# Performance work log

Measured on AMD Instinct MI355X. Metric: run time of the kernel, lower is better.

Reference implementation:

```python
import jax, jax.numpy as jnp
import numpy as np

T, B, E, H, HID, SIG = 1024, 4, 1024, 16, 1024, 64


def setup_inputs() -> dict:
    key = jax.random.key(0)
    ks = jax.random.split(key, 16)
    sc = 0.02
    return {
        "x": jax.random.normal(ks[0], (T, B, E), jnp.float32),
        "Wq": jax.random.normal(ks[1], (E, E), jnp.float32) * sc,
        "bq": jnp.zeros((E,), jnp.float32),
        "Wk": jax.random.normal(ks[2], (E, E), jnp.float32) * sc,
        "bk": jnp.zeros((E,), jnp.float32),
        "Wv": jax.random.normal(ks[3], (E, E), jnp.float32) * sc,
        "bv": jnp.zeros((E,), jnp.float32),
        "Wo": jax.random.normal(ks[4], (E, E), jnp.float32) * sc,
        "bo": jnp.zeros((E,), jnp.float32),
        "W1": jax.random.normal(ks[5], (HID, E), jnp.float32) * sc,
        "b1": jnp.zeros((HID,), jnp.float32),
        "W2": jax.random.normal(ks[6], (SIG, HID), jnp.float32) * sc,
        "b2": jnp.zeros((SIG,), jnp.float32),
        "head_signatures": jax.random.normal(ks[7], (H, SIG), jnp.float32),
    }


def reference(x, Wq, bq, Wk, bk, Wv, bv, Wo, bo, W1, b1, W2, b2, head_signatures):
    # x: (T, B, E) fairseq layout; self-attention, no mask, eval mode (no dropout)
    T_, B_, E_ = x.shape
    H_ = head_signatures.shape[0]
    d = E_ // H_
    scaling = d ** -0.5

    q = (x @ Wq.T + bq) * scaling            # (T,B,E)
    k = x @ Wk.T + bk
    v = x @ Wv.T + bv

    def split_heads(z):                        # (T,B,E) -> (B,H,T,d)
        return z.reshape(T_, B_, H_, d).transpose(1, 2, 0, 3)

    qh, kh, vh = split_heads(q), split_heads(k), split_heads(v)

    scores = jnp.einsum("bhtd,bhsd->bhts", qh, kh)   # (B,H,T,T)
    attn = jax.nn.softmax(scores, axis=-1)
    o = jnp.einsum("bhts,bhsd->bhtd", attn, vh)      # (B,H,T,d)

    # head-competition gate: signature MLP on x, match against head signatures,
    # softmax over heads ('softmax' competition type)
    t = jax.nn.relu(x @ W1.T + b1) @ W2.T + b2       # (T,B,SIG)
    logits = t @ head_signatures.T                   # (T,B,H)
    gate = jax.nn.softmax(logits, axis=-1)
    gate = gate.transpose(1, 2, 0)                   # (B,H,T)

    o = o * gate[..., None]                          # gate per-head outputs
    out = o.transpose(2, 0, 1, 3).reshape(T_, B_, E_)  # (T,B,E)
    return out @ Wo.T + bo
```

## Files before the change

### kernel.cpp

```cpp
#include <hip/hip_runtime.h>

#define Tn   1024
#define Bn   4
#define En   1024
#define Hn   16
#define HIDn 1024
#define SIGn 64
#define Mn   (Tn * Bn)

typedef short  s8x8  __attribute__((ext_vector_type(8)));
typedef float  f32x4 __attribute__((ext_vector_type(4)));

__device__ __forceinline__ unsigned short f2bf(float f) {
    unsigned int x = __float_as_uint(f);
    unsigned int r = (x + 0x7fffu + ((x >> 16) & 1u)) >> 16;
    return (unsigned short)r;
}
__device__ __forceinline__ float exp2asm(float x) {
    float r;
    asm("v_exp_f32 %0, %1" : "=v"(r) : "v"(x));
    return r;
}
__device__ __forceinline__ unsigned int cvtpk(float a, float b) {
    unsigned int r;
    asm("v_cvt_pk_bf16_f32 %0, %1, %2" : "=v"(r) : "v"(a), "v"(b));
    return r;
}

__device__ __forceinline__ void gload_lds16(const void* g, void* l) {
    __builtin_amdgcn_global_load_lds(
        (const __attribute__((address_space(1))) unsigned int*)g,
        (__attribute__((address_space(3))) unsigned int*)l, 16, 0, 0);
}

__device__ __forceinline__ void cast8(const float* s, unsigned short* d) {
    const float4* p = (const float4*)s;
    float4 a = p[0], b = p[1];
    s8x8 o;
    o[0] = (short)f2bf(a.x); o[1] = (short)f2bf(a.y);
    o[2] = (short)f2bf(a.z); o[3] = (short)f2bf(a.w);
    o[4] = (short)f2bf(b.x); o[5] = (short)f2bf(b.y);
    o[6] = (short)f2bf(b.z); o[7] = (short)f2bf(b.w);
    *(s8x8*)d = o;
}

__global__ __launch_bounds__(256) void prep_all(
    const float* __restrict__ x,  const float* __restrict__ W1,
    const float* __restrict__ Wq, const float* __restrict__ Wk,
    const float* __restrict__ Wv, const float* __restrict__ W2,
    const float* __restrict__ b1, const float* __restrict__ bq,
    const float* __restrict__ bk, const float* __restrict__ bv,
    unsigned short* __restrict__ Wcat, unsigned short* __restrict__ W2b,
    float* __restrict__ bcat, unsigned short* __restrict__ xb, int pre)
{
    const size_t WELEM = (size_t)En * En;
    const int y = blockIdx.y, bx = blockIdx.x, tid = threadIdx.x;
    if (y < 4) {
        const float* src = (y == 0) ? W1 : (y == 1) ? Wq : (y == 2) ? Wk : Wv;
        size_t i = (size_t)bx * 256 + tid;
        cast8(src + i * 8, Wcat + y * WELEM + i * 8);
    } else if (y == 4) {
        if (bx < 32) {
            size_t i = (size_t)bx * 256 + tid;
            cast8(W2 + i * 8, W2b + i * 8);
        } else if (bx < 48) {
            int idx = (bx - 32) * 256 + tid;
            int w = idx >> 10;
            const float* s = (w == 0) ? b1 : (w == 1) ? bq : (w == 2) ? bk : bv;
            bcat[idx] = s[idx & 1023];
        }
    } else {
        if (!pre) return;
        int q = y - 5;
        size_t i = (size_t)bx * 256 + tid;
        cast8(x + q * WELEM + i * 8, xb + q * WELEM + i * 8);
    }
}

template <int PRE>
__global__ __launch_bounds__(256) void fused_proj(
    const float* __restrict__ X, const unsigned short* __restrict__ Xb,
    const unsigned short* __restrict__ Wcat, const float* __restrict__ bcat,
    unsigned short* __restrict__ t1b, unsigned short* __restrict__ qb,
    unsigned short* __restrict__ kb, unsigned short* __restrict__ vb)
{
    __shared__ __align__(16) short As[128 * 32];
    __shared__ __align__(16) short Bs[128 * 32];
    const int tid  = threadIdx.x;
    const int wave = tid >> 6;
    const int lane = tid & 63;
    const int ln15 = lane & 15;
    const int kq   = lane >> 4;
    const int wr   = wave >> 1;
    const int wc   = wave & 1;
    const int bn   = blockIdx.x;
    const int bm   = blockIdx.y;
    const size_t rowA0 = (size_t)bm * 128;
    const size_t rowB0 = (size_t)bn * 128;

    const int lrow   = lane >> 2;
    const int lchunk = lane & 3;

    f32x4 acc[4][4];
#pragma unroll
    for (int m = 0; m < 4; m++)
#pragma unroll
        for (int n = 0; n < 4; n++) acc[m][n] = (f32x4){0.f, 0.f, 0.f, 0.f};

    for (int k0 = 0; k0 < 1024; k0 += 32) {
#pragma unroll
        for (int i = 0; i < 2; i++) {
            int row = wave * 32 + i * 16 + lrow;
            int c   = lchunk ^ ((row >> 1) & 3);
            gload_lds16(Wcat + (rowB0 + row) * 1024 + k0 + c * 8,
                        &Bs[(wave * 32 + i * 16) * 32]);
        }
        if (PRE) {
#pragma unroll
            for (int i = 0; i < 2; i++) {
                int row = wave * 32 + i * 16 + lrow;
                int c   = lchunk ^ ((row >> 1) & 3);
                gload_lds16(Xb + (rowA0 + row) * 1024 + k0 + c * 8,
                            &As[(wave * 32 + i * 16) * 32]);
            }
        } else {
            const int srow = tid >> 1;
            const int scol = (tid & 1) * 16;
            const float4* src = (const float4*)(X + (rowA0 + srow) * 1024 + k0 + scol);
            float4 a = src[0], b = src[1], c4 = src[2], d4 = src[3];
            s8x8 v0, v1;
            v0[0] = (short)f2bf(a.x);  v0[1] = (short)f2bf(a.y);
            v0[2] = (short)f2bf(a.z);  v0[3] = (short)f2bf(a.w);
            v0[4] = (short)f2bf(b.x);  v0[5] = (short)f2bf(b.y);
            v0[6] = (short)f2bf(b.z);  v0[7] = (short)f2bf(b.w);
            v1[0] = (short)f2bf(c4.x); v1[1] = (short)f2bf(c4.y);
            v1[2] = (short)f2bf(c4.z); v1[3] = (short)f2bf(c4.w);
            v1[4] = (short)f2bf(d4.x); v1[5] = (short)f2bf(d4.y);
            v1[6] = (short)f2bf(d4.z); v1[7] = (short)f2bf(d4.w);
            int sw = (srow >> 1) & 3;
            int c0 = (scol >> 3) ^ sw;
            int c1 = ((scol >> 3) + 1) ^ sw;
            *(s8x8*)&As[srow * 32 + c0 * 8] = v0;
            *(s8x8*)&As[srow * 32 + c1 * 8] = v1;
        }
        asm volatile("s_waitcnt vmcnt(0)" ::: "memory");
        __syncthreads();

        s8x8 af[4], bf[4];
#pragma unroll
        for (int m = 0; m < 4; m++) {
            int row = wr * 64 + m * 16 + ln15;
            af[m] = *(const s8x8*)&As[row * 32 + (kq ^ ((row >> 1) & 3)) * 8];
        }
#pragma unroll
        for (int n = 0; n < 4; n++) {
            int row = wc * 64 + n * 16 + ln15;
            bf[n] = *(const s8x8*)&Bs[row * 32 + (kq ^ ((row >> 1) & 3)) * 8];
        }
#pragma unroll
        for (int m = 0; m < 4; m++)
#pragma unroll
            for (int n = 0; n < 4; n++)
                acc[m][n] = __builtin_amdgcn_mfma_f32_16x16x32_bf16(
                    af[m], bf[n], acc[m][n], 0, 0, 0);
        __syncthreads();
    }

    const int which = bn >> 3;
    unsigned short* dst = (which == 0) ? t1b : (which == 1) ? qb
                        : (which == 2) ? kb : vb;
    const float scale = (which == 1) ? 0.18033688011112042f : 1.0f;
    const int   relu  = (which == 0);
    const int   cbase = (bn & 7) * 128;

    float bcol[4];
#pragma unroll
    for (int n = 0; n < 4; n++)
        bcol[n] = bcat[bn * 128 + wc * 64 + n * 16 + ln15];
#pragma unroll
    for (int m = 0; m < 4; m++) {
        size_t gr0 = rowA0 + wr * 64 + m * 16 + kq * 4;
#pragma unroll
        for (int n = 0; n < 4; n++) {
            int gc = cbase + wc * 64 + n * 16 + ln15;
#pragma unroll
            for (int j = 0; j < 4; j++) {
                float vv = acc[m][n][j] + bcol[n];
                if (relu) vv = fmaxf(vv, 0.f);
                vv *= scale;
                dst[(gr0 + j) * 1024 + gc] = f2bf(vv);
            }
        }
    }
}

__global__ __launch_bounds__(256) void out_proj(
    const unsigned short* __restrict__ A, const unsigned short* __restrict__ W,
    const float* __restrict__ bias, float* __restrict__ C)
{
    __shared__ __align__(16) short As[64 * 32];
    __shared__ __align__(16) short Bs[128 * 32];
    const int tid  = threadIdx.x;
    const int wave = tid >> 6;
    const int lane = tid & 63;
    const int ln15 = lane & 15;
    const int kq   = lane >> 4;
    const int wr   = wave >> 1;
    const int wc   = wave & 1;
    const size_t rowA0 = (size_t)blockIdx.y * 64;
    const size_t rowB0 = (size_t)blockIdx.x * 128;

    const int lrow   = lane >> 2;
    const int lchunk = lane & 3;

    f32x4 acc[2][4];
#pragma unroll
    for (int m = 0; m < 2; m++)
#pragma unroll
        for (int n = 0; n < 4; n++) acc[m][n] = (f32x4){0.f, 0.f, 0.f, 0.f};

    for (int k0 = 0; k0 < 1024; k0 += 32) {
        {
            int row = wave * 16 + lrow;
            int c   = lchunk ^ ((row >> 1) & 3);
            gload_lds16(A + (rowA0 + row) * 1024 + k0 + c * 8,
                        &As[(wave * 16) * 32]);
        }
#pragma unroll
        for (int i = 0; i < 2; i++) {
            int row = wave * 32 + i * 16 + lrow;
            int c   = lchunk ^ ((row >> 1) & 3);
            gload_lds16(W + (rowB0 + row) * 1024 + k0 + c * 8,
                        &Bs[(wave * 32 + i * 16) * 32]);
        }
        asm volatile("s_waitcnt vmcnt(0)" ::: "memory");
        __syncthreads();

        s8x8 af[2], bf[4];
#pragma unroll
        for (int m = 0; m < 2; m++) {
            int row = wr * 32 + m * 16 + ln15;
            af[m] = *(const s8x8*)&As[row * 32 + (kq ^ ((row >> 1) & 3)) * 8];
        }
#pragma unroll
        for (int n = 0; n < 4; n++) {
            int row = wc * 64 + n * 16 + ln15;
            bf[n] = *(const s8x8*)&Bs[row * 32 + (kq ^ ((row >> 1) & 3)) * 8];
        }
#pragma unroll
        for (int m = 0; m < 2; m++)
#pragma unroll
            for (int n = 0; n < 4; n++)
                acc[m][n] = __builtin_amdgcn_mfma_f32_16x16x32_bf16(
                    af[m], bf[n], acc[m][n], 0, 0, 0);
        __syncthreads();
    }

    float bcol[4];
#pragma unroll
    for (int n = 0; n < 4; n++)
        bcol[n] = bias[rowB0 + wc * 64 + n * 16 + ln15];
#pragma unroll
    for (int m = 0; m < 2; m++) {
        size_t gr0 = rowA0 + wr * 32 + m * 16 + kq * 4;
#pragma unroll
        for (int n = 0; n < 4; n++) {
            size_t gc = rowB0 + wc * 64 + n * 16 + ln15;
#pragma unroll
            for (int j = 0; j < 4; j++)
                C[(gr0 + j) * 1024 + gc] = acc[m][n][j] + bcol[n];
        }
    }
}

__global__ __launch_bounds__(256) void t2gate(
    const unsigned short* __restrict__ t1, const unsigned short* __restrict__ W2b,
    const float* __restrict__ b2, const float* __restrict__ hs,
    float* __restrict__ gate)
{
    __shared__ __align__(16) short As[16 * 64];
    __shared__ __align__(16) short Bs[64 * 64];
    __shared__ float t2s[16][65];
    __shared__ float hss[16][65];
    const int tid   = threadIdx.x;
    const int wave  = tid >> 6;
    const int lane  = tid & 63;
    const int ln15  = lane & 15;
    const int kq    = lane >> 4;
    const int lrow8 = lane >> 3;
    const int lch   = lane & 7;
    const int m0    = blockIdx.x * 16;

    {
        int r = tid >> 4, c = (tid & 15) * 4;
        float4 v = *(const float4*)(hs + r * 64 + c);
        hss[r][c] = v.x; hss[r][c + 1] = v.y; hss[r][c + 2] = v.z; hss[r][c + 3] = v.w;
    }

    f32x4 acc = (f32x4){0.f, 0.f, 0.f, 0.f};
    for (int k0 = 0; k0 < 1024; k0 += 64) {
        if (wave < 2) {
            int row = wave * 8 + lrow8;
            int cg  = lch ^ (row & 7);
            gload_lds16(t1 + (size_t)(m0 + row) * 1024 + k0 + cg * 8,
                        &As[(wave * 8) * 64]);
        }
#pragma unroll
        for (int i = 0; i < 2; i++) {
            int row = wave * 16 + i * 8 + lrow8;
            int cg  = lch ^ (row & 7);
            gload_lds16(W2b + (size_t)row * 1024 + k0 + cg * 8,
                        &Bs[(wave * 16 + i * 8) * 64]);
        }
        asm volatile("s_waitcnt vmcnt(0)" ::: "memory");
        __syncthreads();

#pragma unroll
        for (int kk = 0; kk < 2; kk++) {
            int arow = ln15;
            int brow = wave * 16 + ln15;
            s8x8 af = *(const s8x8*)&As[arow * 64 + (((kk * 4 + kq) ^ (arow & 7)) * 8)];
            s8x8 bf = *(const s8x8*)&Bs[brow * 64 + (((kk * 4 + kq) ^ (brow & 7)) * 8)];
            acc = __builtin_amdgcn_mfma_f32_16x16x32_bf16(af, bf, acc, 0, 0, 0);
        }
        __syncthreads();
    }

#pragma unroll
    for (int j = 0; j < 4; j++)
        t2s[kq * 4 + j][wave * 16 + ln15] = acc[j] + b2[wave * 16 + ln15];
    __syncthreads();

    int r = tid >> 4, hd = tid & 15;
    float s = 0.f;
#pragma unroll 16
    for (int d = 0; d < 64; d++) s += t2s[r][d] * hss[hd][d];
    float mx = s;
    mx = fmaxf(mx, __shfl_xor(mx, 1));
    mx = fmaxf(mx, __shfl_xor(mx, 2));
    mx = fmaxf(mx, __shfl_xor(mx, 4));
    mx = fmaxf(mx, __shfl_xor(mx, 8));
    float e = __expf(s - mx);
    float sum = e;
    sum += __shfl_xor(sum, 1);
    sum += __shfl_xor(sum, 2);
    sum += __shfl_xor(sum, 4);
    sum += __shfl_xor(sum, 8);
    gate[(size_t)(m0 + r) * Hn + hd] = e / sum;
}

__global__ __launch_bounds__(256) void trans_wo(
    const unsigned short* __restrict__ vb, unsigned short* __restrict__ vt,
    const float* __restrict__ Wo, unsigned short* __restrict__ Wob)
{
    const int bx = blockIdx.x, tid = threadIdx.x;
    if (bx >= 1024) {
        size_t i = (size_t)(bx - 1024) * 256 + tid;
        cast8(Wo + i * 8, Wob + i * 8);
        return;
    }
    __shared__ unsigned short ts[64][65];
    const int bh = bx & 63;
    const int b = bh >> 4, h = bh & 15;
    const int t0 = (bx >> 6) * 64;
    {
        int tr = tid >> 2, dq = (tid & 3) * 16;
        const unsigned short* src =
            vb + ((size_t)(t0 + tr) * Bn + b) * En + h * 64 + dq;
        s8x8 a = *(const s8x8*)src;
        s8x8 c = *(const s8x8*)(src + 8);
#pragma unroll
        for (int i = 0; i < 8; i++) {
            ts[tr][dq + i]     = (unsigned short)a[i];
            ts[tr][dq + 8 + i] = (unsigned short)c[i];
        }
    }
    __syncthreads();
    {
        int dr = tid >> 2, tq = (tid & 3) * 16;
        unsigned short* dst = vt + ((size_t)bh * 64 + dr) * Tn + t0 + tq;
        s8x8 o0, o1;
#pragma unroll
        for (int i = 0; i < 8; i++) {
            o0[i] = (short)ts[tq + i][dr];
            o1[i] = (short)ts[tq + 8 + i][dr];
        }
        *(s8x8*)dst = o0;
        *(s8x8*)(dst + 8) = o1;
    }
}

__global__ __launch_bounds__(512, 2) void attn_mfma(
    const unsigned short* __restrict__ q, const unsigned short* __restrict__ k,
    const unsigned short* __restrict__ vt, const float* __restrict__ gate,
    unsigned short* __restrict__ o)
{
    __shared__ __align__(16) short Kls[2][64 * 64];
    __shared__ __align__(16) short Vls[2][64 * 64];

    const int tid  = threadIdx.x;
    const int w    = tid >> 6;
    const int lane = tid & 63;
    const int ln   = lane & 15;
    const int kq   = lane >> 4;
    const int bh   = blockIdx.x;
    const int b    = bh >> 4;
    const int h    = bh & 15;
    const int qt   = blockIdx.y;

    s8x8 qf[2];
    {
        const int qrow = qt * 128 + w * 16 + ln;
        const unsigned short* src =
            q + ((size_t)qrow * Bn + b) * En + h * 64 + kq * 8;
        qf[0] = *(const s8x8*)(src);
        qf[1] = *(const s8x8*)(src + 32);
    }

    f32x4 OT[4];
#pragma unroll
    for (int n = 0; n < 4; n++) OT[n] = (f32x4){0.f, 0.f, 0.f, 0.f};
    float mrun = -1e30f, lrun = 0.f;

    const int srow = w * 8 + (lane >> 3);
    const int sch  = (lane & 7) ^ (srow & 7);
    const int sn  = srow >> 4;
    const int sK0 = 32 * (sn >> 1) + 4 * (sn & 1)
                  + 8 * ((srow >> 2) & 3) + (srow & 3);

    auto stage = [&](int bufi, int s0) {
        const unsigned short* gk =
            k + ((size_t)(s0 + sK0) * Bn + b) * En + h * 64 + sch * 8;
        gload_lds16(gk, &Kls[bufi][w * 512]);
        const unsigned short* gv =
            vt + ((size_t)bh * 64 + srow) * Tn + s0 + sch * 8;
        gload_lds16(gv, &Vls[bufi][w * 512]);
    };

    stage(0, 0);
    asm volatile("s_waitcnt vmcnt(0)" ::: "memory");
    __syncthreads();

    int cur = 0;
    for (int t = 0; t < Tn / 64; t++) {
        if (t + 1 < Tn / 64) stage(cur ^ 1, (t + 1) * 64);

        f32x4 S[4];
        __builtin_amdgcn_s_setprio(1);
#pragma unroll
        for (int n = 0; n < 4; n++) {
            S[n] = (f32x4){0.f, 0.f, 0.f, 0.f};
#pragma unroll
            for (int kk = 0; kk < 2; kk++) {
                int row = n * 16 + ln;
                int cc  = (kk * 4 + kq) ^ (row & 7);
                s8x8 kf = *(const s8x8*)&Kls[cur][row * 64 + cc * 8];
                S[n] = __builtin_amdgcn_mfma_f32_16x16x32_bf16(kf, qf[kk], S[n], 0, 0, 0);
            }
        }
        __builtin_amdgcn_s_setprio(0);

        float rm;
        {
            f32x4 t0 = S[0];
#pragma unroll
            for (int n = 1; n < 4; n++) {
                t0[0] = fmaxf(t0[0], S[n][0]); t0[1] = fmaxf(t0[1], S[n][1]);
                t0[2] = fmaxf(t0[2], S[n][2]); t0[3] = fmaxf(t0[3], S[n][3]);
            }
            rm = fmaxf(fmaxf(t0[0], t0[1]), fmaxf(t0[2], t0[3]));
            rm = fmaxf(rm, __shfl_xor(rm, 16));
            rm = fmaxf(rm, __shfl_xor(rm, 32));
        }

        if (__any(rm > mrun + 8.0f)) {
            float mnew = fmaxf(mrun, rm);
            float fs = exp2asm(mrun - mnew);
            lrun *= fs;
#pragma unroll
            for (int n = 0; n < 4; n++) {
                OT[n][0] *= fs; OT[n][1] *= fs; OT[n][2] *= fs; OT[n][3] *= fs;
            }
            mrun = mnew;
        }

        float ps = 0.f;
#pragma unroll
        for (int n = 0; n < 4; n++) {
            S[n][0] = exp2asm(S[n][0] - mrun); ps += S[n][0];
            S[n][1] = exp2asm(S[n][1] - mrun); ps += S[n][1];
            S[n][2] = exp2asm(S[n][2] - mrun); ps += S[n][2];
            S[n][3] = exp2asm(S[n][3] - mrun); ps += S[n][3];
        }
        ps += __shfl_xor(ps, 16);
        ps += __shfl_xor(ps, 32);
        lrun += ps;

        union { unsigned int u[4]; s8x8 v; } pb[2];
#pragma unroll
        for (int kk = 0; kk < 2; kk++) {
            pb[kk].u[0] = cvtpk(S[2 * kk][0],     S[2 * kk][1]);
            pb[kk].u[1] = cvtpk(S[2 * kk][2],     S[2 * kk][3]);
            pb[kk].u[2] = cvtpk(S[2 * kk + 1][0], S[2 * kk + 1][1]);
            pb[kk].u[3] = cvtpk(S[2 * kk + 1][2], S[2 * kk + 1][3]);
        }

        __builtin_amdgcn_s_setprio(1);
#pragma unroll
        for (int kk = 0; kk < 2; kk++) {
#pragma unroll
            for (int n = 0; n < 4; n++) {
                int row = n * 16 + ln;
                int cv  = (kk * 4 + kq) ^ (row & 7);
                s8x8 vf = *(const s8x8*)&Vls[cur][row * 64 + cv * 8];
                OT[n] = __builtin_amdgcn_mfma_f32_16x16x32_bf16(vf, pb[kk].v, OT[n], 0, 0, 0);
            }
        }
        __builtin_amdgcn_s_setprio(0);

        asm volatile("s_waitcnt vmcnt(0)" ::: "memory");
        __syncthreads();
        cur ^= 1;
    }

    {
        int tq = qt * 128 + w * 16 + ln;
        size_t m = (size_t)tq * Bn + b;
        float g = gate[m * Hn + h] / lrun;
        unsigned short* dst = o + m * En + h * 64;
#pragma unroll
        for (int n = 0; n < 4; n++) {
            int d0 = n * 16 + kq * 4;
            uint2 pkv;
            pkv.x = cvtpk(OT[n][0] * g, OT[n][1] * g);
            pkv.y = cvtpk(OT[n][2] * g, OT[n][3] * g);
            *(uint2*)(dst + d0) = pkv;
        }
    }
}

extern "C" void kernel_launch(void* const* d_in, const int* in_sizes, int n_in,
                              void* d_out, int out_size, void* d_ws, size_t ws_size,
                              hipStream_t stream)
{
    const float* x  = (const float*)d_in[0];
    const float* Wq = (const float*)d_in[1];
    const float* bq = (const float*)d_in[2];
    const float* Wk = (const float*)d_in[3];
    const float* bk = (const float*)d_in[4];
    const float* Wv = (const float*)d_in[5];
    const float* bv = (const float*)d_in[6];
    const float* Wo = (const float*)d_in[7];
    const float* bo = (const float*)d_in[8];
    const float* W1 = (const float*)d_in[9];
    const float* b1 = (const float*)d_in[10];
    const float* W2 = (const float*)d_in[11];
    const float* b2 = (const float*)d_in[12];
    const float* hs = (const float*)d_in[13];

    const size_t WELEM = (size_t)En * En;
    unsigned short* Wcat = (unsigned short*)d_ws;
    unsigned short* W2b  = Wcat + 4 * WELEM;
    float* bcat = (float*)(W2b + (size_t)SIGn * HIDn);
    float* gate = bcat + 4096;
    unsigned short* t1b = (unsigned short*)(gate + (size_t)Mn * Hn);
    unsigned short* qb  = t1b + (size_t)Mn * En;
    unsigned short* kb  = qb  + (size_t)Mn * En;
    unsigned short* vb  = kb  + (size_t)Mn * En;
    unsigned short* xb  = vb  + (size_t)Mn * En;
    unsigned short* Wob = Wcat;
    unsigned short* vtb = t1b;
    unsigned short* ob  = vb;

    const size_t need_xb =
        (size_t)((char*)(xb + (size_t)Mn * En) - (char*)d_ws);
    const bool pre = ws_size >= need_xb;

    dim3 blk(256);

    prep_all<<<dim3(512, 9), blk, 0, stream>>>(
        x, W1, Wq, Wk, Wv, W2, b1, bq, bk, bv, Wcat, W2b, bcat, xb, (int)pre);

    if (pre) {
        fused_proj<1><<<dim3(32, 32), blk, 0, stream>>>(
            x, xb, Wcat, bcat, t1b, qb, kb, vb);
    } else {
        fused_proj<0><<<dim3(32, 32), blk, 0, stream>>>(
            x, xb, Wcat, bcat, t1b, qb, kb, vb);
    }

    t2gate<<<dim3(Mn / 16), blk, 0, stream>>>(t1b, W2b, b2, hs, gate);

    trans_wo<<<dim3(1536), blk, 0, stream>>>(vb, vtb, Wo, Wob);

    attn_mfma<<<dim3(Bn * Hn, Tn / 128), dim3(512), 0, stream>>>(
        qb, kb, vtb, gate, ob);

    out_proj<<<dim3(En / 128, Mn / 64), blk, 0, stream>>>(ob, Wob, bo, (float*)d_out);
}
```

Measured before the change: 124.3 us.

## Pipeline projection GEMM with per-wave double-buffered LDS and merge mid-stage kernels

```diff
diff --git a/kernel.cpp b/kernel.cpp
--- a/kernel.cpp
+++ b/kernel.cpp
@@ -77,9 +77,136 @@
     }
 }
 
-template <int PRE>
-__global__ __launch_bounds__(256) void fused_proj(
-    const float* __restrict__ X, const unsigned short* __restrict__ Xb,
+__global__ __launch_bounds__(256) void fused_proj_pipe(
+    const unsigned short* __restrict__ Xb,
+    const unsigned short* __restrict__ Wcat, const float* __restrict__ bcat,
+    unsigned short* __restrict__ t1b, unsigned short* __restrict__ qb,
+    unsigned short* __restrict__ kb, unsigned short* __restrict__ vb)
+{
+    __shared__ __align__(16) short Ls[4][2][2][64 * 32];
+    const int tid  = threadIdx.x;
+    const int wave = tid >> 6;
+    const int lane = tid & 63;
+    const int ln15 = lane & 15;
+    const int kq   = lane >> 4;
+    const int wr   = wave >> 1;
+    const int wc   = wave & 1;
+    const int bn   = blockIdx.x;
+    const int bm   = blockIdx.y;
+    const size_t rowA0 = (size_t)bm * 128;
+    const size_t rowB0 = (size_t)bn * 128;
+
+    const int lr = lane >> 2;
+    const int lc = lane & 3;
+    const unsigned short* pa[4];
+    const unsigned short* pb[4];
+#pragma unroll
+    for (int i = 0; i < 4; i++) {
+        int r = i * 16 + lr;
+        int c = lc ^ ((r >> 1) & 3);
+        pa[i] = Xb   + (rowA0 + wr * 64 + r) * 1024 + c * 8;
+        pb[i] = Wcat + (rowB0 + wc * 64 + r) * 1024 + c * 8;
+    }
+    short* lA0 = &Ls[wave][0][0][0];
+    short* lA1 = &Ls[wave][1][0][0];
+    short* lB0 = &Ls[wave][0][1][0];
+    short* lB1 = &Ls[wave][1][1][0];
+
+    f32x4 acc[4][4];
+#pragma unroll
+    for (int m = 0; m < 4; m++)
+#pragma unroll
+        for (int n = 0; n < 4; n++) acc[m][n] = (f32x4){0.f, 0.f, 0.f, 0.f};
+
+    const int rsw = (kq ^ ((ln15 >> 1) & 3)) * 8;
+
+#define STAGE(lA, lB)                                          \
+    do {                                                       \
+        _Pragma("unroll")                                      \
+        for (int i = 0; i < 4; i++)                            \
+            gload_lds16(pa[i], (lA) + i * 16 * 32);            \
+        _Pragma("unroll")                                      \
+        for (int i = 0; i < 4; i++)                            \
+            gload_lds16(pb[i], (lB) + i * 16 * 32);            \
+        _Pragma("unroll")                                      \
+        for (int i = 0; i < 4; i++) { pa[i] += 32; pb[i] += 32; } \
+    } while (0)
+
+#define COMPUTE(lA, lB)                                                   \
+    do {                                                                  \
+        s8x8 af[4], bf4[4];                                               \
+        _Pragma("unroll")                                                 \
+        for (int m = 0; m < 4; m++)                                       \
+            af[m] = *(const s8x8*)((lA) + (m * 16 + ln15) * 32 + rsw);    \
+        _Pragma("unroll")                                                 \
+        for (int n = 0; n < 4; n++)                                       \
+            bf4[n] = *(const s8x8*)((lB) + (n * 16 + ln15) * 32 + rsw);   \
+        _Pragma("unroll")                                                 \
+        for (int m = 0; m < 4; m++)                                       \
+            _Pragma("unroll")                                             \
+            for (int n = 0; n < 4; n++)                                   \
+                acc[m][n] = __builtin_amdgcn_mfma_f32_16x16x32_bf16(      \
+                    af[m], bf4[n], acc[m][n], 0, 0, 0);                   \
+    } while (0)
+
+    STAGE(lA0, lB0);
+    STAGE(lA1, lB1);
+
+    for (int t = 0; t < 28; t += 2) {
+        asm volatile("s_waitcnt vmcnt(8)" ::: "memory");
+        COMPUTE(lA0, lB0);
+        asm volatile("s_waitcnt lgkmcnt(0)" ::: "memory");
+        STAGE(lA0, lB0);
+        asm volatile("s_waitcnt vmcnt(8)" ::: "memory");
+        COMPUTE(lA1, lB1);
+        asm volatile("s_waitcnt lgkmcnt(0)" ::: "memory");
+        STAGE(lA1, lB1);
+    }
+    asm volatile("s_waitcnt vmcnt(8)" ::: "memory");
+    COMPUTE(lA0, lB0);
+    asm volatile("s_waitcnt lgkmcnt(0)" ::: "memory");
+    STAGE(lA0, lB0);
+    asm volatile("s_waitcnt vmcnt(8)" ::: "memory");
+    COMPUTE(lA1, lB1);
+    asm volatile("s_waitcnt lgkmcnt(0)" ::: "memory");
+    STAGE(lA1, lB1);
+    asm volatile("s_waitcnt vmcnt(8)" ::: "memory");
+    COMPUTE(lA0, lB0);
+    asm volatile("s_waitcnt vmcnt(0)" ::: "memory");
+    COMPUTE(lA1, lB1);
+#undef STAGE
+#undef COMPUTE
+
+    const int which = bn >> 3;
+    unsigned short* dst = (which == 0) ? t1b : (which == 1) ? qb
+                        : (which == 2) ? kb : vb;
+    const float scale = (which == 1) ? 0.18033688011112042f : 1.0f;
+    const int   relu  = (which == 0);
+    const int   cbase = (bn & 7) * 128;
+
+    float bcol[4];
+#pragma unroll
+    for (int n = 0; n < 4; n++)
+        bcol[n] = bcat[bn * 128 + wc * 64 + n * 16 + ln15];
+#pragma unroll
+    for (int m = 0; m < 4; m++) {
+        size_t gr0 = rowA0 + wr * 64 + m * 16 + kq * 4;
+#pragma unroll
+        for (int n = 0; n < 4; n++) {
+            int gc = cbase + wc * 64 + n * 16 + ln15;
+#pragma unroll
+            for (int j = 0; j < 4; j++) {
+                float vv = acc[m][n][j] + bcol[n];
+                if (relu) vv = fmaxf(vv, 0.f);
+                vv *= scale;
+                dst[(gr0 + j) * 1024 + gc] = f2bf(vv);
+            }
+        }
+    }
+}
+
+__global__ __launch_bounds__(256) void fused_proj_fb(
+    const float* __restrict__ X,
     const unsigned short* __restrict__ Wcat, const float* __restrict__ bcat,
     unsigned short* __restrict__ t1b, unsigned short* __restrict__ qb,
     unsigned short* __restrict__ kb, unsigned short* __restrict__ vb)
@@ -97,7 +224,6 @@
     const int bm   = blockIdx.y;
     const size_t rowA0 = (size_t)bm * 128;
     const size_t rowB0 = (size_t)bn * 128;
-
     const int lrow   = lane >> 2;
     const int lchunk = lane & 3;
 
@@ -115,15 +241,7 @@
             gload_lds16(Wcat + (rowB0 + row) * 1024 + k0 + c * 8,
                         &Bs[(wave * 32 + i * 16) * 32]);
         }
-        if (PRE) {
-#pragma unroll
-            for (int i = 0; i < 2; i++) {
-                int row = wave * 32 + i * 16 + lrow;
-                int c   = lchunk ^ ((row >> 1) & 3);
-                gload_lds16(Xb + (rowA0 + row) * 1024 + k0 + c * 8,
-                            &As[(wave * 32 + i * 16) * 32]);
-            }
-        } else {
+        {
             const int srow = tid >> 1;
             const int scol = (tid & 1) * 16;
             const float4* src = (const float4*)(X + (rowA0 + srow) * 1024 + k0 + scol);
@@ -209,7 +327,6 @@
     const int wc   = wave & 1;
     const size_t rowA0 = (size_t)blockIdx.y * 64;
     const size_t rowB0 = (size_t)blockIdx.x * 128;
-
     const int lrow   = lane >> 2;
     const int lchunk = lane & 3;
 
@@ -273,23 +390,20 @@
     }
 }
 
-__global__ __launch_bounds__(256) void t2gate(
+__device__ __forceinline__ void t2gate_body(
+    int blk, int tid,
     const unsigned short* __restrict__ t1, const unsigned short* __restrict__ W2b,
     const float* __restrict__ b2, const float* __restrict__ hs,
-    float* __restrict__ gate)
-{
-    __shared__ __align__(16) short As[16 * 64];
-    __shared__ __align__(16) short Bs[64 * 64];
-    __shared__ float t2s[16][65];
-    __shared__ float hss[16][65];
-    const int tid   = threadIdx.x;
+    float* __restrict__ gate,
+    short* As, short* Bs, float (*t2s)[65], float (*hss)[65])
+{
     const int wave  = tid >> 6;
     const int lane  = tid & 63;
     const int ln15  = lane & 15;
     const int kq    = lane >> 4;
     const int lrow8 = lane >> 3;
     const int lch   = lane & 7;
-    const int m0    = blockIdx.x * 16;
+    const int m0    = blk * 16;
 
     {
         int r = tid >> 4, c = (tid & 15) * 4;
@@ -303,14 +417,14 @@
             int row = wave * 8 + lrow8;
             int cg  = lch ^ (row & 7);
             gload_lds16(t1 + (size_t)(m0 + row) * 1024 + k0 + cg * 8,
-                        &As[(wave * 8) * 64]);
+                        As + (wave * 8) * 64);
         }
 #pragma unroll
         for (int i = 0; i < 2; i++) {
             int row = wave * 16 + i * 8 + lrow8;
             int cg  = lch ^ (row & 7);
             gload_lds16(W2b + (size_t)row * 1024 + k0 + cg * 8,
-                        &Bs[(wave * 16 + i * 8) * 64]);
+                        Bs + (wave * 16 + i * 8) * 64);
         }
         asm volatile("s_waitcnt vmcnt(0)" ::: "memory");
         __syncthreads();
@@ -319,8 +433,8 @@
         for (int kk = 0; kk < 2; kk++) {
             int arow = ln15;
             int brow = wave * 16 + ln15;
-            s8x8 af = *(const s8x8*)&As[arow * 64 + (((kk * 4 + kq) ^ (arow & 7)) * 8)];
-            s8x8 bf = *(const s8x8*)&Bs[brow * 64 + (((kk * 4 + kq) ^ (brow & 7)) * 8)];
+            s8x8 af = *(const s8x8*)(As + arow * 64 + (((kk * 4 + kq) ^ (arow & 7)) * 8));
+            s8x8 bf = *(const s8x8*)(Bs + brow * 64 + (((kk * 4 + kq) ^ (brow & 7)) * 8));
             acc = __builtin_amdgcn_mfma_f32_16x16x32_bf16(af, bf, acc, 0, 0, 0);
         }
         __syncthreads();
@@ -349,20 +463,12 @@
     gate[(size_t)(m0 + r) * Hn + hd] = e / sum;
 }
 
-__global__ __launch_bounds__(256) void trans_wo(
+__device__ __forceinline__ void vtrans_body(
+    int bh, int t0, int tid,
     const unsigned short* __restrict__ vb, unsigned short* __restrict__ vt,
-    const float* __restrict__ Wo, unsigned short* __restrict__ Wob)
-{
-    const int bx = blockIdx.x, tid = threadIdx.x;
-    if (bx >= 1024) {
-        size_t i = (size_t)(bx - 1024) * 256 + tid;
-        cast8(Wo + i * 8, Wob + i * 8);
-        return;
-    }
-    __shared__ unsigned short ts[64][65];
-    const int bh = bx & 63;
+    unsigned short (*ts)[65])
+{
     const int b = bh >> 4, h = bh & 15;
-    const int t0 = (bx >> 6) * 64;
     {
         int tr = tid >> 2, dq = (tid & 3) * 16;
         const unsigned short* src =
@@ -387,6 +493,55 @@
         }
         *(s8x8*)dst = o0;
         *(s8x8*)(dst + 8) = o1;
+    }
+}
+
+__global__ __launch_bounds__(256) void t2gate_k(
+    const unsigned short* __restrict__ t1, const unsigned short* __restrict__ W2b,
+    const float* __restrict__ b2, const float* __restrict__ hs,
+    float* __restrict__ gate)
+{
+    __shared__ __align__(16) short As[16 * 64];
+    __shared__ __align__(16) short Bs[64 * 64];
+    __shared__ float t2s[16][65];
+    __shared__ float hss[16][65];
+    t2gate_body(blockIdx.x, threadIdx.x, t1, W2b, b2, hs, gate, As, Bs, t2s, hss);
+}
+__global__ __launch_bounds__(256) void trans_wo_k(
+    const unsigned short* __restrict__ vb, unsigned short* __restrict__ vt,
+    const float* __restrict__ Wo, unsigned short* __restrict__ Wob)
+{
+    const int bx = blockIdx.x, tid = threadIdx.x;
+    if (bx >= 1024) {
+        size_t i = (size_t)(bx - 1024) * 256 + tid;
+        cast8(Wo + i * 8, Wob + i * 8);
+        return;
+    }
+    __shared__ unsigned short ts[64][65];
+    vtrans_body(bx & 63, (bx >> 6) * 64, tid, vb, vt, ts);
+}
+
+__global__ __launch_bounds__(256) void midstage(
+    const unsigned short* __restrict__ t1, const unsigned short* __restrict__ W2b,
+    const float* __restrict__ b2, const float* __restrict__ hs,
+    float* __restrict__ gate,
+    const unsigned short* __restrict__ vb, unsigned short* __restrict__ vt,
+    const float* __restrict__ Wo, unsigned short* __restrict__ Wob)
+{
+    __shared__ __align__(16) short As[16 * 64];
+    __shared__ __align__(16) short Bs[64 * 64];
+    __shared__ float t2s[16][65];
+    __shared__ float hss[16][65];
+    __shared__ unsigned short ts[64][65];
+    const int bx = blockIdx.x, tid = threadIdx.x;
+    if (bx < 256) {
+        t2gate_body(bx, tid, t1, W2b, b2, hs, gate, As, Bs, t2s, hss);
+    } else if (bx < 1280) {
+        int v = bx - 256;
+        vtrans_body(v & 63, (v >> 6) * 64, tid, vb, vt, ts);
+    } else {
+        size_t i = (size_t)(bx - 1280) * 256 + tid;
+        cast8(Wo + i * 8, Wob + i * 8);
     }
 }
 
@@ -569,7 +724,6 @@
     unsigned short* vb  = kb  + (size_t)Mn * En;
     unsigned short* xb  = vb  + (size_t)Mn * En;
     unsigned short* Wob = Wcat;
-    unsigned short* vtb = t1b;
     unsigned short* ob  = vb;
 
     const size_t need_xb =
@@ -582,19 +736,22 @@
         x, W1, Wq, Wk, Wv, W2, b1, bq, bk, bv, Wcat, W2b, bcat, xb, (int)pre);
 
     if (pre) {
-        fused_proj<1><<<dim3(32, 32), blk, 0, stream>>>(
-            x, xb, Wcat, bcat, t1b, qb, kb, vb);
+        unsigned short* vtb = xb;
+        fused_proj_pipe<<<dim3(32, 32), blk, 0, stream>>>(
+            xb, Wcat, bcat, t1b, qb, kb, vb);
+        midstage<<<dim3(1792), blk, 0, stream>>>(
+            t1b, W2b, b2, hs, gate, vb, vtb, Wo, Wob);
+        attn_mfma<<<dim3(Bn * Hn, Tn / 128), dim3(512), 0, stream>>>(
+            qb, kb, vtb, gate, ob);
     } else {
-        fused_proj<0><<<dim3(32, 32), blk, 0, stream>>>(
-            x, xb, Wcat, bcat, t1b, qb, kb, vb);
-    }
-
-    t2gate<<<dim3(Mn / 16), blk, 0, stream>>>(t1b, W2b, b2, hs, gate);
-
-    trans_wo<<<dim3(1536), blk, 0, stream>>>(vb, vtb, Wo, Wob);
-
-    attn_mfma<<<dim3(Bn * Hn, Tn / 128), dim3(512), 0, stream>>>(
-        qb, kb, vtb, gate, ob);
+        unsigned short* vtb = t1b;
+        fused_proj_fb<<<dim3(32, 32), blk, 0, stream>>>(
+            x, Wcat, bcat, t1b, qb, kb, vb);
+        t2gate_k<<<dim3(Mn / 16), blk, 0, stream>>>(t1b, W2b, b2, hs, gate);
+        trans_wo_k<<<dim3(1536), blk, 0, stream>>>(vb, vtb, Wo, Wob);
+        attn_mfma<<<dim3(Bn * Hn, Tn / 128), dim3(512), 0, stream>>>(
+            qb, kb, vtb, gate, ob);
+    }
 
     out_proj<<<dim3(En / 128, Mn / 64), blk, 0, stream>>>(ob, Wob, bo, (float*)d_out);
 }
```

New measurement: 128.2 us. 3.1% more time.
